# Kernel optimization log

Measured on AMD Instinct MI355X. Metric: run time of the kernel, lower is better.

Reference implementation:

```python
import jax, jax.numpy as jnp
import numpy as np
import functools, math

HEADS = 16


def _query_chunk_attention(query, key, value, precision, key_chunk_size=4096):
    # query: (q_chunk, bh, d); key/value: (kv, bh, d)
    num_kv, num_heads, k_features = key.shape[-3:]
    v_features = value.shape[-1]
    key_chunk_size = min(key_chunk_size, num_kv)
    query = query / jnp.sqrt(k_features)

    @functools.partial(jax.checkpoint, prevent_cse=False)
    def summarize_chunk(query, key, value):
        attn_weights = jnp.einsum("...qhd,...khd->...qhk", query, key, precision=precision)
        max_score = jnp.max(attn_weights, axis=-1, keepdims=True)
        max_score = jax.lax.stop_gradient(max_score)
        exp_weights = jnp.exp(attn_weights - max_score)
        exp_values = jnp.einsum("...vhf,...qhv->...qhf", value, exp_weights, precision=precision)
        max_score = jnp.einsum("...qhk->...qh", max_score)
        return exp_values, exp_weights.sum(axis=-1), max_score

    def chunk_scanner(chunk_idx):
        key_chunk = jax.lax.dynamic_slice(
            key, [chunk_idx, 0, 0], [key_chunk_size, num_heads, k_features])
        value_chunk = jax.lax.dynamic_slice(
            value, [chunk_idx, 0, 0], [key_chunk_size, num_heads, v_features])
        return summarize_chunk(query, key_chunk, value_chunk)

    chunk_values, chunk_weights, chunk_max = jax.lax.map(
        chunk_scanner, xs=jnp.arange(0, num_kv, key_chunk_size))
    # online softmax rescaling across kv chunks
    global_max = jnp.max(chunk_max, axis=0, keepdims=True)
    max_diffs = jnp.exp(chunk_max - global_max)
    chunk_values = chunk_values * jnp.expand_dims(max_diffs, axis=-1)
    chunk_weights = chunk_weights * max_diffs
    all_values = chunk_values.sum(axis=0)
    all_weights = jnp.expand_dims(chunk_weights, -1).sum(axis=0)
    return all_values / all_weights


def jax_memory_efficient_attention(query, key, value,
                                   precision=jax.lax.Precision.HIGHEST,
                                   query_chunk_size=1024, key_chunk_size=4096):
    # query: (q_len, bh, d)
    num_q, num_heads, q_features = query.shape[-3:]

    def chunk_scanner(chunk_idx, _):
        query_chunk = jax.lax.dynamic_slice(
            query, [chunk_idx, 0, 0],
            [min(query_chunk_size, num_q), num_heads, q_features])
        return (chunk_idx + query_chunk_size,
                _query_chunk_attention(query_chunk, key, value, precision, key_chunk_size))

    _, res = jax.lax.scan(chunk_scanner, 0, xs=None,
                          length=math.ceil(num_q / query_chunk_size))
    return jnp.concatenate(res, axis=-3)


def _reshape_heads_to_batch_dim(tensor, heads):
    b, s, d = tensor.shape
    t = tensor.reshape(b, s, heads, d // heads).transpose(0, 2, 1, 3)
    return t.reshape(b * heads, s, d // heads)


def _attention_fwd(query, key, value):
    heads = HEADS
    q = _reshape_heads_to_batch_dim(query, heads).transpose(1, 0, 2)  # (s, b*h, dh)
    k = _reshape_heads_to_batch_dim(key, heads).transpose(1, 0, 2)
    v = _reshape_heads_to_batch_dim(value, heads).transpose(1, 0, 2)
    flatten_latent_dim = q.shape[-3]
    if flatten_latent_dim % 64 == 0:
        query_chunk_size = flatten_latent_dim // 64
    elif flatten_latent_dim % 16 == 0:
        query_chunk_size = flatten_latent_dim // 16
    elif flatten_latent_dim % 4 == 0:
        query_chunk_size = flatten_latent_dim // 4
    else:
        query_chunk_size = flatten_latent_dim
    out = jax_memory_efficient_attention(q, k, v,
                                         query_chunk_size=query_chunk_size,
                                         key_chunk_size=4096 * 4)
    return out.transpose(1, 0, 2)  # (b*h, s, dh)


def setup_inputs() -> dict:
    key = jax.random.key(0)
    k1, k2, k3 = jax.random.split(key, 3)
    B, S, D = 2, 4096, 1024
    return {
        "query": jax.random.normal(k1, (B, S, D), dtype=jnp.float32),
        "key": jax.random.normal(k2, (B, S, D), dtype=jnp.float32),
        "value": jax.random.normal(k3, (B, S, D), dtype=jnp.float32),
    }


def reference(query, key, value):
    return _attention_fwd(query, key, value)
```

## Files before the change

kernel.cpp:

```cpp
#include <hip/hip_runtime.h>
#include <math.h>

#define SEQ    4096
#define DH     64
#define DMODEL 1024
#define NBH    32
#define QT     256
#define KTS    128
#define NTS    (SEQ / KTS)
#define LOG2E  1.44269504088896340736f

typedef __attribute__((ext_vector_type(8)))  short short8;
typedef __attribute__((ext_vector_type(4)))  float f32x4;
typedef __attribute__((ext_vector_type(16))) float f32x16;
typedef __attribute__((ext_vector_type(4)))  int   int4v;
typedef __attribute__((ext_vector_type(2)))  unsigned uint2v;

__device__ __forceinline__ unsigned short f2bf(float f) {
  union { float f; unsigned u; } x; x.f = f;
  unsigned r = x.u + 0x7FFFu + ((x.u >> 16) & 1u);
  return (unsigned short)(r >> 16);
}

__device__ __forceinline__ unsigned cvtpk_bf16(float lo, float hi) {
  unsigned r;
  asm("v_cvt_pk_bf16_f32 %0, %1, %2" : "=v"(r) : "v"(lo), "v"(hi));
  return r;
}

__global__ __launch_bounds__(256)
void prep(const float* __restrict__ Kp, const float* __restrict__ Vp,
          unsigned short* __restrict__ ws) {
  __shared__ unsigned short Kt[KTS * DH];
  __shared__ unsigned short Vt[KTS * DH];
  const int blk = blockIdx.x;
  const int bh = blk >> 5, t = blk & 31;
  const int b = bh >> 4, h = bh & 15;
  const size_t gbase = (size_t)b * SEQ * DMODEL + (size_t)h * DH +
                       (size_t)t * KTS * DMODEL;
  const float* Kb = Kp + gbase;
  const float* Vb = Vp + gbase;
  unsigned short* wt = ws + (size_t)blk * 16384;
  const int tid = threadIdx.x;

#pragma unroll
  for (int c = 0; c < 8; ++c) {
    const int idx = c * 256 + tid;
    const int row = idx >> 4, dc = idx & 15;
    f32x4 kf = *(const f32x4*)(Kb + (size_t)row * DMODEL + dc * 4);
    f32x4 vf = *(const f32x4*)(Vb + (size_t)row * DMODEL + dc * 4);
    uint2v ku, vu;
    ku[0] = (unsigned)f2bf(kf[0]) | ((unsigned)f2bf(kf[1]) << 16);
    ku[1] = (unsigned)f2bf(kf[2]) | ((unsigned)f2bf(kf[3]) << 16);
    vu[0] = (unsigned)f2bf(vf[0]) | ((unsigned)f2bf(vf[1]) << 16);
    vu[1] = (unsigned)f2bf(vf[2]) | ((unsigned)f2bf(vf[3]) << 16);
    *(uint2v*)&Kt[row * 64 + dc * 4] = ku;
    *(uint2v*)&Vt[row * 64 + dc * 4] = vu;
  }
  __syncthreads();

#pragma unroll
  for (int c = 0; c < 4; ++c) {
    const int idx = c * 256 + tid;
    const int l31 = idx & 31, hi = (idx >> 5) & 1, d4 = (idx >> 6) & 3, kb = idx >> 8;
    short8 v = *(const short8*)&Kt[(kb * 32 + l31) * 64 + d4 * 16 + hi * 8];
    *(short8*)&wt[idx * 8] = v;
  }
#pragma unroll
  for (int c = 0; c < 4; ++c) {
    const int idx = c * 256 + tid;
    const int l31 = idx & 31, dt = (idx >> 5) & 1, hi = (idx >> 6) & 1, k16 = idx >> 7;
    const int d = dt * 32 + l31, kb0 = k16 * 16 + hi * 8;
    short8 v;
#pragma unroll
    for (int j = 0; j < 8; ++j) v[j] = (short)Vt[(kb0 + j) * 64 + d];
    *(short8*)&wt[8192 + idx * 8] = v;
  }
}

__global__ __launch_bounds__(512, 4)
void fattn(const float* __restrict__ Qp,
           const unsigned short* __restrict__ ws,
           float* __restrict__ Op) {
  __shared__ __align__(16) int4v lds4[2][2048];

  const int tid  = threadIdx.x;
  const int lane = tid & 63;
  const int w    = tid >> 6;
  const int hi   = lane >> 5;
  const int l31  = lane & 31;

  const int id  = blockIdx.x;
  const int rid = (id & 7) * 64 + (id >> 3);
  const int bh  = rid >> 4;
  const int qt  = rid & 15;
  const int q0  = qt * QT + w * 32;

  const int b = bh >> 4, h = bh & 15;
  const float* Qb = Qp + (size_t)b * SEQ * DMODEL + (size_t)h * DH;
  const unsigned short* wsb = ws + (size_t)bh * NTS * 16384;

  short8 qb[4];
  {
    const float* qr = Qb + (size_t)(q0 + l31) * DMODEL;
    const float s = 0.125f * LOG2E;
#pragma unroll
    for (int d4 = 0; d4 < 4; ++d4) {
      const float* p = qr + d4 * 16 + hi * 8;
      f32x4 f0 = *(const f32x4*)p;
      f32x4 f1 = *(const f32x4*)(p + 4);
      short8 v;
#pragma unroll
      for (int i = 0; i < 4; ++i) {
        v[i]     = (short)f2bf(f0[i] * s);
        v[i + 4] = (short)f2bf(f1[i] * s);
      }
      qb[d4] = v;
    }
  }

  f32x16 acc[2];
#pragma unroll
  for (int dt = 0; dt < 2; ++dt)
#pragma unroll
    for (int r = 0; r < 16; ++r) acc[dt][r] = 0.f;
  float lsum = 0.f;

  const int laneK = hi * 512 + l31 * 16;
  const int laneV = hi * 1024 + l31 * 16;
  const char* ldsB = (const char*)lds4;

  {
    const int4v* src = (const int4v*)wsb;
#pragma unroll
    for (int c = 0; c < 4; ++c) lds4[0][c * 512 + tid] = src[c * 512 + tid];
  }
  __syncthreads();

  for (int t = 0; t < NTS; ++t) {
    const int buf = t & 1;
    const int bufo = buf << 15;
    int4v st0, st1, st2, st3;
    const bool pf = (t + 1 < NTS);
    if (pf) {
      const int4v* src = (const int4v*)(wsb + (size_t)(t + 1) * 16384);
      st0 = src[0 * 512 + tid];
      st1 = src[1 * 512 + tid];
      st2 = src[2 * 512 + tid];
      st3 = src[3 * 512 + tid];
    }

#pragma unroll
    for (int kb = 0; kb < 4; ++kb) {
      short8 ka[4];
#pragma unroll
      for (int d4 = 0; d4 < 4; ++d4)
        ka[d4] = *(const short8*)(ldsB + bufo + kb * 4096 + d4 * 1024 + laneK);
      f32x16 z;
#pragma unroll
      for (int r = 0; r < 16; ++r) z[r] = 0.f;
      __builtin_amdgcn_s_setprio(1);
      z = __builtin_amdgcn_mfma_f32_32x32x16_bf16(ka[0], qb[0], z, 0, 0, 0);
      z = __builtin_amdgcn_mfma_f32_32x32x16_bf16(ka[1], qb[1], z, 0, 0, 0);
      z = __builtin_amdgcn_mfma_f32_32x32x16_bf16(ka[2], qb[2], z, 0, 0, 0);
      z = __builtin_amdgcn_mfma_f32_32x32x16_bf16(ka[3], qb[3], z, 0, 0, 0);
      __builtin_amdgcn_s_setprio(0);

#pragma unroll
      for (int r = 0; r < 16; ++r) z[r] = __builtin_amdgcn_exp2f(z[r]);
      {
        float s0 = (z[0] + z[1]) + (z[2] + z[3]);
        float s1 = (z[4] + z[5]) + (z[6] + z[7]);
        float s2 = (z[8] + z[9]) + (z[10] + z[11]);
        float s3 = (z[12] + z[13]) + (z[14] + z[15]);
        lsum += (s0 + s1) + (s2 + s3);
      }

#pragma unroll
      for (int s = 0; s < 2; ++s) {
        const int R = 8 * s;
        unsigned a0 = cvtpk_bf16(z[R + 0], z[R + 1]);
        unsigned b0 = cvtpk_bf16(z[R + 4], z[R + 5]);
        unsigned a1 = cvtpk_bf16(z[R + 2], z[R + 3]);
        unsigned b1 = cvtpk_bf16(z[R + 6], z[R + 7]);
        asm("v_permlane32_swap_b32 %0, %1" : "+v"(a0), "+v"(b0));
        asm("v_permlane32_swap_b32 %0, %1" : "+v"(a1), "+v"(b1));
        union { unsigned u[4]; short8 s8; } pw;
        pw.u[0] = a0; pw.u[1] = a1; pw.u[2] = b0; pw.u[3] = b1;
        const int k16 = kb * 2 + s;
        __builtin_amdgcn_s_setprio(1);
#pragma unroll
        for (int dt = 0; dt < 2; ++dt) {
          short8 vb = *(const short8*)(ldsB + bufo + 16384 + k16 * 2048 +
                                       dt * 512 + laneV);
          acc[dt] = __builtin_amdgcn_mfma_f32_32x32x16_bf16(pw.s8, vb, acc[dt], 0, 0, 0);
        }
        __builtin_amdgcn_s_setprio(0);
      }
    }

    if (pf) {
      int4v* dst = &lds4[buf ^ 1][0];
      dst[0 * 512 + tid] = st0;
      dst[1 * 512 + tid] = st1;
      dst[2 * 512 + tid] = st2;
      dst[3 * 512 + tid] = st3;
    }
    __syncthreads();
  }

  const float lt  = lsum + __shfl_xor(lsum, 32, 64);
  const float inv = 1.0f / lt;
#pragma unroll
  for (int dt = 0; dt < 2; ++dt)
#pragma unroll
    for (int r = 0; r < 16; ++r) {
      const int qrow = (r & 3) + 8 * (r >> 2) + 4 * hi;
      const float iv = __shfl(inv, qrow + (lane & 32), 64);
      const size_t row = (size_t)bh * SEQ + q0 + qrow;
      Op[row * DH + dt * 32 + l31] = acc[dt][r] * iv;
    }
}

extern "C" void kernel_launch(void* const* d_in, const int* in_sizes, int n_in,
                              void* d_out, int out_size, void* d_ws, size_t ws_size,
                              hipStream_t stream) {
  const float* Q = (const float*)d_in[0];
  const float* K = (const float*)d_in[1];
  const float* V = (const float*)d_in[2];
  float* O = (float*)d_out;
  unsigned short* ws = (unsigned short*)d_ws;

  prep<<<dim3(NBH * NTS), dim3(256), 0, stream>>>(K, V, ws);
  fattn<<<dim3(512), dim3(512), 0, stream>>>(Q, ws, O);
}
```

Measured before the change: 159.3 us.

## Give each wave two query tiles and stage K/V via direct global-to-LDS loads

Each wave now handles 64 query rows as two 32-row subtiles, so every K and V fragment read from LDS feeds two MFMAs. The block shrinks from 8 to 4 waves while still covering 256 queries. The register-staged prefetch of the next K/V tile is replaced by global_load_lds, which copies straight into the other LDS buffer and frees the VGPRs used for staging. The cost is twice the accumulator and score registers per wave, plus fewer waves per block to hide latency.

```diff
diff --git a/kernel.cpp b/kernel.cpp
--- a/kernel.cpp
+++ b/kernel.cpp
@@ -5,7 +5,6 @@
 #define DH     64
 #define DMODEL 1024
 #define NBH    32
-#define QT     256
 #define KTS    128
 #define NTS    (SEQ / KTS)
 #define LOG2E  1.44269504088896340736f
@@ -13,7 +12,6 @@
 typedef __attribute__((ext_vector_type(8)))  short short8;
 typedef __attribute__((ext_vector_type(4)))  float f32x4;
 typedef __attribute__((ext_vector_type(16))) float f32x16;
-typedef __attribute__((ext_vector_type(4)))  int   int4v;
 typedef __attribute__((ext_vector_type(2)))  unsigned uint2v;
 
 __device__ __forceinline__ unsigned short f2bf(float f) {
@@ -78,11 +76,11 @@
   }
 }
 
-__global__ __launch_bounds__(512, 4)
+__global__ __launch_bounds__(256, 2)
 void fattn(const float* __restrict__ Qp,
            const unsigned short* __restrict__ ws,
            float* __restrict__ Op) {
-  __shared__ __align__(16) int4v lds4[2][2048];
+  __shared__ __align__(16) char lds[2][32768];
 
   const int tid  = threadIdx.x;
   const int lane = tid & 63;
@@ -94,16 +92,17 @@
   const int rid = (id & 7) * 64 + (id >> 3);
   const int bh  = rid >> 4;
   const int qt  = rid & 15;
-  const int q0  = qt * QT + w * 32;
+  const int q0  = qt * 256 + w * 64;
 
   const int b = bh >> 4, h = bh & 15;
   const float* Qb = Qp + (size_t)b * SEQ * DMODEL + (size_t)h * DH;
-  const unsigned short* wsb = ws + (size_t)bh * NTS * 16384;
-
-  short8 qb[4];
-  {
-    const float* qr = Qb + (size_t)(q0 + l31) * DMODEL;
-    const float s = 0.125f * LOG2E;
+  const char* wsb = (const char*)(ws + (size_t)bh * NTS * 16384);
+
+  short8 qb[2][4];
+#pragma unroll
+  for (int s = 0; s < 2; ++s) {
+    const float* qr = Qb + (size_t)(q0 + s * 32 + l31) * DMODEL;
+    const float sc = 0.125f * LOG2E;
 #pragma unroll
     for (int d4 = 0; d4 < 4; ++d4) {
       const float* p = qr + d4 * 16 + hi * 8;
@@ -112,114 +111,134 @@
       short8 v;
 #pragma unroll
       for (int i = 0; i < 4; ++i) {
-        v[i]     = (short)f2bf(f0[i] * s);
-        v[i + 4] = (short)f2bf(f1[i] * s);
-      }
-      qb[d4] = v;
+        v[i]     = (short)f2bf(f0[i] * sc);
+        v[i + 4] = (short)f2bf(f1[i] * sc);
+      }
+      qb[s][d4] = v;
     }
   }
 
-  f32x16 acc[2];
-#pragma unroll
-  for (int dt = 0; dt < 2; ++dt)
-#pragma unroll
-    for (int r = 0; r < 16; ++r) acc[dt][r] = 0.f;
-  float lsum = 0.f;
+  f32x16 ZERO;
+#pragma unroll
+  for (int r = 0; r < 16; ++r) ZERO[r] = 0.f;
+
+  f32x16 acc[2][2];
+#pragma unroll
+  for (int s = 0; s < 2; ++s)
+#pragma unroll
+    for (int dt = 0; dt < 2; ++dt) acc[s][dt] = ZERO;
+  float lsum[2] = {0.f, 0.f};
 
   const int laneK = hi * 512 + l31 * 16;
   const int laneV = hi * 1024 + l31 * 16;
-  const char* ldsB = (const char*)lds4;
-
-  {
-    const int4v* src = (const int4v*)wsb;
-#pragma unroll
-    for (int c = 0; c < 4; ++c) lds4[0][c * 512 + tid] = src[c * 512 + tid];
-  }
+
+#define STAGE(buf_, t_)                                                       \
+  {                                                                           \
+    const char* src_ = wsb + (size_t)(t_) * 32768;                            \
+    char* dst_ = &lds[buf_][0];                                               \
+    _Pragma("unroll")                                                         \
+    for (int c_ = 0; c_ < 8; ++c_) {                                          \
+      __builtin_amdgcn_global_load_lds(                                       \
+          (const __attribute__((address_space(1))) void*)(src_ + c_ * 4096 +  \
+                                                          w * 1024 + lane * 16), \
+          (__attribute__((address_space(3))) void*)(dst_ + c_ * 4096 +        \
+                                                    w * 1024),                \
+          16, 0, 0);                                                          \
+    }                                                                         \
+  }
+
+  STAGE(0, 0);
   __syncthreads();
 
   for (int t = 0; t < NTS; ++t) {
     const int buf = t & 1;
-    const int bufo = buf << 15;
-    int4v st0, st1, st2, st3;
-    const bool pf = (t + 1 < NTS);
-    if (pf) {
-      const int4v* src = (const int4v*)(wsb + (size_t)(t + 1) * 16384);
-      st0 = src[0 * 512 + tid];
-      st1 = src[1 * 512 + tid];
-      st2 = src[2 * 512 + tid];
-      st3 = src[3 * 512 + tid];
-    }
+    if (t + 1 < NTS) STAGE(buf ^ 1, t + 1);
+    const char* Lk = &lds[buf][0];
+    const char* Lv = &lds[buf][16384];
 
 #pragma unroll
     for (int kb = 0; kb < 4; ++kb) {
       short8 ka[4];
 #pragma unroll
       for (int d4 = 0; d4 < 4; ++d4)
-        ka[d4] = *(const short8*)(ldsB + bufo + kb * 4096 + d4 * 1024 + laneK);
-      f32x16 z;
-#pragma unroll
-      for (int r = 0; r < 16; ++r) z[r] = 0.f;
+        ka[d4] = *(const short8*)(Lk + kb * 4096 + d4 * 1024 + laneK);
+      f32x16 zA, zB;
       __builtin_amdgcn_s_setprio(1);
-      z = __builtin_amdgcn_mfma_f32_32x32x16_bf16(ka[0], qb[0], z, 0, 0, 0);
-      z = __builtin_amdgcn_mfma_f32_32x32x16_bf16(ka[1], qb[1], z, 0, 0, 0);
-      z = __builtin_amdgcn_mfma_f32_32x32x16_bf16(ka[2], qb[2], z, 0, 0, 0);
-      z = __builtin_amdgcn_mfma_f32_32x32x16_bf16(ka[3], qb[3], z, 0, 0, 0);
+      zA = __builtin_amdgcn_mfma_f32_32x32x16_bf16(ka[0], qb[0][0], ZERO, 0, 0, 0);
+      zB = __builtin_amdgcn_mfma_f32_32x32x16_bf16(ka[0], qb[1][0], ZERO, 0, 0, 0);
+      zA = __builtin_amdgcn_mfma_f32_32x32x16_bf16(ka[1], qb[0][1], zA, 0, 0, 0);
+      zB = __builtin_amdgcn_mfma_f32_32x32x16_bf16(ka[1], qb[1][1], zB, 0, 0, 0);
+      zA = __builtin_amdgcn_mfma_f32_32x32x16_bf16(ka[2], qb[0][2], zA, 0, 0, 0);
+      zB = __builtin_amdgcn_mfma_f32_32x32x16_bf16(ka[2], qb[1][2], zB, 0, 0, 0);
+      zA = __builtin_amdgcn_mfma_f32_32x32x16_bf16(ka[3], qb[0][3], zA, 0, 0, 0);
+      zB = __builtin_amdgcn_mfma_f32_32x32x16_bf16(ka[3], qb[1][3], zB, 0, 0, 0);
       __builtin_amdgcn_s_setprio(0);
 
 #pragma unroll
-      for (int r = 0; r < 16; ++r) z[r] = __builtin_amdgcn_exp2f(z[r]);
+      for (int r = 0; r < 16; ++r) zA[r] = __builtin_amdgcn_exp2f(zA[r]);
+#pragma unroll
+      for (int r = 0; r < 16; ++r) zB[r] = __builtin_amdgcn_exp2f(zB[r]);
       {
-        float s0 = (z[0] + z[1]) + (z[2] + z[3]);
-        float s1 = (z[4] + z[5]) + (z[6] + z[7]);
-        float s2 = (z[8] + z[9]) + (z[10] + z[11]);
-        float s3 = (z[12] + z[13]) + (z[14] + z[15]);
-        lsum += (s0 + s1) + (s2 + s3);
+        float a0 = (zA[0] + zA[1]) + (zA[2] + zA[3]);
+        float a1 = (zA[4] + zA[5]) + (zA[6] + zA[7]);
+        float a2 = (zA[8] + zA[9]) + (zA[10] + zA[11]);
+        float a3 = (zA[12] + zA[13]) + (zA[14] + zA[15]);
+        lsum[0] += (a0 + a1) + (a2 + a3);
+        float b0 = (zB[0] + zB[1]) + (zB[2] + zB[3]);
+        float b1 = (zB[4] + zB[5]) + (zB[6] + zB[7]);
+        float b2 = (zB[8] + zB[9]) + (zB[10] + zB[11]);
+        float b3 = (zB[12] + zB[13]) + (zB[14] + zB[15]);
+        lsum[1] += (b0 + b1) + (b2 + b3);
       }
 
 #pragma unroll
       for (int s = 0; s < 2; ++s) {
         const int R = 8 * s;
-        unsigned a0 = cvtpk_bf16(z[R + 0], z[R + 1]);
-        unsigned b0 = cvtpk_bf16(z[R + 4], z[R + 5]);
-        unsigned a1 = cvtpk_bf16(z[R + 2], z[R + 3]);
-        unsigned b1 = cvtpk_bf16(z[R + 6], z[R + 7]);
-        asm("v_permlane32_swap_b32 %0, %1" : "+v"(a0), "+v"(b0));
-        asm("v_permlane32_swap_b32 %0, %1" : "+v"(a1), "+v"(b1));
-        union { unsigned u[4]; short8 s8; } pw;
-        pw.u[0] = a0; pw.u[1] = a1; pw.u[2] = b0; pw.u[3] = b1;
+        unsigned a0 = cvtpk_bf16(zA[R + 0], zA[R + 1]);
+        unsigned c0 = cvtpk_bf16(zA[R + 4], zA[R + 5]);
+        unsigned a1 = cvtpk_bf16(zA[R + 2], zA[R + 3]);
+        unsigned c1 = cvtpk_bf16(zA[R + 6], zA[R + 7]);
+        asm("v_permlane32_swap_b32 %0, %1" : "+v"(a0), "+v"(c0));
+        asm("v_permlane32_swap_b32 %0, %1" : "+v"(a1), "+v"(c1));
+        union { unsigned u[4]; short8 s8; } pwA;
+        pwA.u[0] = a0; pwA.u[1] = a1; pwA.u[2] = c0; pwA.u[3] = c1;
+        unsigned d0 = cvtpk_bf16(zB[R + 0], zB[R + 1]);
+        unsigned e0 = cvtpk_bf16(zB[R + 4], zB[R + 5]);
+        unsigned d1 = cvtpk_bf16(zB[R + 2], zB[R + 3]);
+        unsigned e1 = cvtpk_bf16(zB[R + 6], zB[R + 7]);
+        asm("v_permlane32_swap_b32 %0, %1" : "+v"(d0), "+v"(e0));
+        asm("v_permlane32_swap_b32 %0, %1" : "+v"(d1), "+v"(e1));
+        union { unsigned u[4]; short8 s8; } pwB;
+        pwB.u[0] = d0; pwB.u[1] = d1; pwB.u[2] = e0; pwB.u[3] = e1;
+
         const int k16 = kb * 2 + s;
+        short8 vb0 = *(const short8*)(Lv + k16 * 2048 + laneV);
+        short8 vb1 = *(const short8*)(Lv + k16 * 2048 + 512 + laneV);
         __builtin_amdgcn_s_setprio(1);
-#pragma unroll
-        for (int dt = 0; dt < 2; ++dt) {
-          short8 vb = *(const short8*)(ldsB + bufo + 16384 + k16 * 2048 +
-                                       dt * 512 + laneV);
-          acc[dt] = __builtin_amdgcn_mfma_f32_32x32x16_bf16(pw.s8, vb, acc[dt], 0, 0, 0);
-        }
+        acc[0][0] = __builtin_amdgcn_mfma_f32_32x32x16_bf16(pwA.s8, vb0, acc[0][0], 0, 0, 0);
+        acc[0][1] = __builtin_amdgcn_mfma_f32_32x32x16_bf16(pwA.s8, vb1, acc[0][1], 0, 0, 0);
+        acc[1][0] = __builtin_amdgcn_mfma_f32_32x32x16_bf16(pwB.s8, vb0, acc[1][0], 0, 0, 0);
+        acc[1][1] = __builtin_amdgcn_mfma_f32_32x32x16_bf16(pwB.s8, vb1, acc[1][1], 0, 0, 0);
         __builtin_amdgcn_s_setprio(0);
       }
-    }
-
-    if (pf) {
-      int4v* dst = &lds4[buf ^ 1][0];
-      dst[0 * 512 + tid] = st0;
-      dst[1 * 512 + tid] = st1;
-      dst[2 * 512 + tid] = st2;
-      dst[3 * 512 + tid] = st3;
     }
     __syncthreads();
   }
 
-  const float lt  = lsum + __shfl_xor(lsum, 32, 64);
-  const float inv = 1.0f / lt;
-#pragma unroll
-  for (int dt = 0; dt < 2; ++dt)
-#pragma unroll
-    for (int r = 0; r < 16; ++r) {
-      const int qrow = (r & 3) + 8 * (r >> 2) + 4 * hi;
-      const float iv = __shfl(inv, qrow + (lane & 32), 64);
-      const size_t row = (size_t)bh * SEQ + q0 + qrow;
-      Op[row * DH + dt * 32 + l31] = acc[dt][r] * iv;
-    }
+#pragma unroll
+  for (int s = 0; s < 2; ++s) {
+    const float lt  = lsum[s] + __shfl_xor(lsum[s], 32, 64);
+    const float inv = 1.0f / lt;
+#pragma unroll
+    for (int dt = 0; dt < 2; ++dt)
+#pragma unroll
+      for (int r = 0; r < 16; ++r) {
+        const int qrow = (r & 3) + 8 * (r >> 2) + 4 * hi;
+        const float iv = __shfl(inv, qrow + (lane & 32), 64);
+        const size_t row = (size_t)bh * SEQ + q0 + s * 32 + qrow;
+        Op[row * DH + dt * 32 + l31] = acc[s][dt][r] * iv;
+      }
+  }
 }
 
 extern "C" void kernel_launch(void* const* d_in, const int* in_sizes, int n_in,
@@ -232,5 +251,5 @@
   unsigned short* ws = (unsigned short*)d_ws;
 
   prep<<<dim3(NBH * NTS), dim3(256), 0, stream>>>(K, V, ws);
-  fattn<<<dim3(512), dim3(512), 0, stream>>>(Q, ws, O);
-}
+  fattn<<<dim3(512), dim3(256), 0, stream>>>(Q, ws, O);
+}
```

After: 155.2 us. -2.6%, faster.
